# Performance work log

Measured on AMD Instinct MI355X. Metric: run time of the kernel, lower is better.

The kernel has to match this reference:

```python
import jax, jax.numpy as jnp
import numpy as np

_EPS = 1e-12  # torch F.normalize eps


def _normalize(x):
    # x: [B, N, 3]; matches torch.nn.functional.normalize(x, dim=2)
    norm = jnp.linalg.norm(x, axis=2, keepdims=True)
    return x / jnp.maximum(norm, _EPS)


def setup_inputs() -> dict:
    key = jax.random.key(0)
    k1, k2 = jax.random.split(key)
    xyz1 = jax.random.normal(k1, (8, 4096, 6), dtype=jnp.float32)
    xyz2 = jax.random.normal(k2, (8, 4096, 6), dtype=jnp.float32)
    return {"xyz1": xyz1, "xyz2": xyz2}


def reference(xyz1, xyz2):
    p1 = xyz1[:, :, :3]  # [B, N, 3]
    p2 = xyz2[:, :, :3]  # [B, M, 3]
    n1 = xyz1[:, :, 3:]  # [B, N, 3]
    n2 = xyz2[:, :, 3:]  # [B, M, 3]

    # Pairwise squared L2: |a|^2 + |b|^2 - 2 a.b  -> [B, N, M]
    sq1 = jnp.sum(p1 * p1, axis=2)  # [B, N]
    sq2 = jnp.sum(p2 * p2, axis=2)  # [B, M]
    cross = jnp.einsum('bnd,bmd->bnm', p1, p2)
    d = sq1[:, :, None] + sq2[:, None, :] - 2.0 * cross  # [B, N, M]

    dist1 = jnp.min(d, axis=2)      # [B, N] NN of each p1 in p2
    idx1 = jnp.argmin(d, axis=2)    # [B, N]
    dist2 = jnp.min(d, axis=1)      # [B, M] NN of each p2 in p1
    idx2 = jnp.argmin(d, axis=1)    # [B, M]

    # Gather matched normals
    t1 = jnp.take_along_axis(n2, idx1[:, :, None], axis=1)  # [B, N, 3]
    t2 = jnp.take_along_axis(n1, idx2[:, :, None], axis=1)  # [B, M, 3]

    nd1 = jnp.sum((_normalize(n1) - _normalize(t1)) ** 2, axis=2)  # [B, N]
    nd2 = jnp.sum((_normalize(n2) - _normalize(t2)) ** 2, axis=2)  # [B, M]

    return jnp.mean(dist1) + jnp.mean(dist2) + jnp.mean(nd1) + jnp.mean(nd2)
```

## Files before the change

### kernel.cpp

```cpp
#include <hip/hip_runtime.h>
#include <cstdint>

#define NB 8
#define NP 4096
#define NDB 16
#define THREADS 256
#define Q 8
#define CHUNK (THREADS * Q)
#define NCHUNK (NP / CHUNK)
#define SEG 64
#define TSEG (NP / SEG)


__global__ __launch_bounds__(256) void chamfer_prep(
    const float* __restrict__ xyz1, const float* __restrict__ xyz2,
    float4* __restrict__ pk, float4* __restrict__ nrm)
{
    int gid = blockIdx.x * 256 + threadIdx.x;
    int c = gid >> 15;
    const float* src = (c ? xyz2 : xyz1) + (size_t)(gid & 32767) * 6;
    const float2* s2 = (const float2*)src;
    float2 a = s2[0], bv = s2[1], cv = s2[2];
    float x = a.x, y = a.y, z = bv.x;
    float nx = bv.y, ny = cv.x, nz = cv.y;
    pk[gid] = make_float4(x, y, z, -0.5f * (x * x + y * y + z * z));
    float rn = 1.0f / fmaxf(sqrtf(nx * nx + ny * ny + nz * nz), 1e-12f);
    nrm[gid] = make_float4(nx * rn, ny * rn, nz * rn, 0.0f);
}

__global__ __launch_bounds__(THREADS) void chamfer_argmin(
    const float4* __restrict__ pk, float* __restrict__ scores)
{
    __shared__ float4 tgt[TSEG];

    unsigned int x = blockIdx.x;
    int seg   = x & (SEG - 1);
    int chunk = (x >> 6) & (NCHUNK - 1);
    int db    = x >> 7;
    int b     = db & 7;
    int dir   = db >> 3;
    int qrow  = dir * NB + b;
    int trow  = (1 - dir) * NB + b;

    if (threadIdx.x < TSEG)
        tgt[threadIdx.x] = pk[(size_t)trow * NP + seg * TSEG + threadIdx.x];
    __syncthreads();

    const float4* qp = pk + (size_t)qrow * NP;
    float qx[Q], qy[Q], qz[Q], bs[Q];
    int qbase = chunk * CHUNK + threadIdx.x;
    #pragma unroll
    for (int i = 0; i < Q; ++i) {
        float4 qv = qp[qbase + i * THREADS];
        qx[i] = qv.x; qy[i] = qv.y; qz[i] = qv.z;
        bs[i] = -3.4e38f;
    }

    #pragma unroll 8
    for (int k = 0; k < TSEG; ++k) {
        float4 t = tgt[k];
        #pragma unroll
        for (int i = 0; i < Q; ++i) {
            float s = fmaf(t.x, qx[i], fmaf(t.y, qy[i], fmaf(t.z, qz[i], t.w)));
            bs[i] = fmaxf(bs[i], s);
        }
    }

    float* srow = scores + ((size_t)db * SEG + seg) * NP + qbase;
    #pragma unroll
    for (int i = 0; i < Q; ++i) srow[i * THREADS] = bs[i];
}

__global__ __launch_bounds__(256) void chamfer_finish(
    const float4* __restrict__ pk, const float4* __restrict__ nrm,
    const float* __restrict__ scores, float* __restrict__ out)
{
    int gid = blockIdx.x * 256 + threadIdx.x;
    int q  = gid & (NP - 1);
    int db = gid >> 12;
    int b  = db & 7;
    int dir = db >> 3;
    int qrow = dir * NB + b;
    int trow = (1 - dir) * NB + b;

    const float* sb = scores + (size_t)db * SEG * NP + q;
    float best = -3.4e38f;
    int wseg = 0;
    #pragma unroll
    for (int s = 0; s < SEG; ++s) {
        float v = sb[(size_t)s * NP];
        wseg = (v > best) ? s : wseg;
        best = fmaxf(best, v);
    }

    float4 qv = pk[(size_t)qrow * NP + q];
    const float4* tb = pk + (size_t)trow * NP + wseg * TSEG;
    int jf = -1;
    #pragma unroll 8
    for (int k = 0; k < TSEG; ++k) {
        float4 t = tb[k];
        float s = fmaf(t.x, qv.x, fmaf(t.y, qv.y, fmaf(t.z, qv.z, t.w)));
        bool hit = (s == best) && (jf < 0);
        jf = hit ? k : jf;
    }
    int j = wseg * TSEG + (jf < 0 ? 0 : jf);

    float d = fmaxf(-2.0f * (qv.w + best), 0.0f);

    float4 a = nrm[(size_t)qrow * NP + q];
    float4 t = nrm[(size_t)trow * NP + j];
    float dot = a.x * t.x + a.y * t.y + a.z * t.z;
    float nd = fmaf(-2.0f, dot, 2.0f);

    float contrib = (d + nd) * (1.0f / 32768.0f);
    for (int off = 32; off > 0; off >>= 1)
        contrib += __shfl_down(contrib, off, 64);
    __shared__ float wsum[4];
    if ((threadIdx.x & 63) == 0) wsum[threadIdx.x >> 6] = contrib;
    __syncthreads();
    if (threadIdx.x == 0)
        atomicAdd(out, wsum[0] + wsum[1] + wsum[2] + wsum[3]);
}

extern "C" void kernel_launch(void* const* d_in, const int* in_sizes, int n_in,
                              void* d_out, int out_size, void* d_ws, size_t ws_size,
                              hipStream_t stream) {
    const float* xyz1 = (const float*)d_in[0];
    const float* xyz2 = (const float*)d_in[1];
    char* ws = (char*)d_ws;
    float4* pk     = (float4*)(ws);
    float4* nrm    = (float4*)(ws + (1u << 20));
    float*  scores = (float*)(ws + (2u << 20));

    hipMemsetAsync(d_out, 0, sizeof(float), stream);
    chamfer_prep<<<256, 256, 0, stream>>>(xyz1, xyz2, pk, nrm);
    chamfer_argmin<<<NDB * NCHUNK * SEG, THREADS, 0, stream>>>(pk, scores);
    chamfer_finish<<<(NDB * NP) / 256, 256, 0, stream>>>(pk, nrm, scores, (float*)d_out);
}
```

Before: 96.94 us.

## Use packed FP32 FMA over target pairs and widen per-thread query tile

The argmin kernel now handles two target points per step with v_pk_fma_f32. The targets are rearranged in shared memory into x/y/z/w pairs, and each query is duplicated into float2 registers. Each thread now holds 16 queries instead of 8, which halves the grid to one block per (direction, batch, segment) and doubles reuse of each shared-memory load. The output memset is folded into the prep kernel to drop an API call. The change risks higher register pressure, lower occupancy and a smaller grid (1024 blocks), and packed FMA rounding may break exact equality with the finish kernel's scalar recomputation of the best score.

```diff
diff --git a/kernel.cpp b/kernel.cpp
--- a/kernel.cpp
+++ b/kernel.cpp
@@ -5,18 +5,25 @@
 #define NP 4096
 #define NDB 16
 #define THREADS 256
-#define Q 8
-#define CHUNK (THREADS * Q)
-#define NCHUNK (NP / CHUNK)
+#define Q 16
 #define SEG 64
 #define TSEG (NP / SEG)
+#define NPAIR (TSEG / 2)
 
+
+__device__ inline float2 pk_fma(float2 a, float2 b, float2 c) {
+    float2 d;
+    asm("v_pk_fma_f32 %0, %1, %2, %3"
+        : "=v"(d) : "v"(a), "v"(b), "v"(c));
+    return d;
+}
 
 __global__ __launch_bounds__(256) void chamfer_prep(
     const float* __restrict__ xyz1, const float* __restrict__ xyz2,
-    float4* __restrict__ pk, float4* __restrict__ nrm)
+    float4* __restrict__ pk, float4* __restrict__ nrm, float* __restrict__ out)
 {
     int gid = blockIdx.x * 256 + threadIdx.x;
+    if (gid == 0) *out = 0.0f;
     int c = gid >> 15;
     const float* src = (c ? xyz2 : xyz1) + (size_t)(gid & 32767) * 6;
     const float2* s2 = (const float2*)src;
@@ -31,42 +38,55 @@
 __global__ __launch_bounds__(THREADS) void chamfer_argmin(
     const float4* __restrict__ pk, float* __restrict__ scores)
 {
-    __shared__ float4 tgt[TSEG];
+    __shared__ float tgt[TSEG * 4];
 
     unsigned int x = blockIdx.x;
-    int seg   = x & (SEG - 1);
-    int chunk = (x >> 6) & (NCHUNK - 1);
-    int db    = x >> 7;
-    int b     = db & 7;
-    int dir   = db >> 3;
-    int qrow  = dir * NB + b;
-    int trow  = (1 - dir) * NB + b;
+    int seg = x & (SEG - 1);
+    int db  = x >> 6;
+    int b   = db & 7;
+    int dir = db >> 3;
+    int qrow = dir * NB + b;
+    int trow = (1 - dir) * NB + b;
 
-    if (threadIdx.x < TSEG)
-        tgt[threadIdx.x] = pk[(size_t)trow * NP + seg * TSEG + threadIdx.x];
+    if (threadIdx.x < TSEG) {
+        float4 t = pk[(size_t)trow * NP + seg * TSEG + threadIdx.x];
+        int blk = threadIdx.x >> 1, h = threadIdx.x & 1;
+        float* dstp = tgt + blk * 8 + h;
+        dstp[0] = t.x; dstp[2] = t.y; dstp[4] = t.z; dstp[6] = t.w;
+    }
     __syncthreads();
 
     const float4* qp = pk + (size_t)qrow * NP;
-    float qx[Q], qy[Q], qz[Q], bs[Q];
-    int qbase = chunk * CHUNK + threadIdx.x;
+    float2 qx2[Q], qy2[Q], qz2[Q];
+    float bs[Q];
     #pragma unroll
     for (int i = 0; i < Q; ++i) {
-        float4 qv = qp[qbase + i * THREADS];
-        qx[i] = qv.x; qy[i] = qv.y; qz[i] = qv.z;
+        float4 qv = qp[threadIdx.x + i * THREADS];
+        qx2[i] = make_float2(qv.x, qv.x);
+        qy2[i] = make_float2(qv.y, qv.y);
+        qz2[i] = make_float2(qv.z, qv.z);
         bs[i] = -3.4e38f;
     }
 
-    #pragma unroll 8
-    for (int k = 0; k < TSEG; ++k) {
-        float4 t = tgt[k];
+    const float4* tp = (const float4*)tgt;
+    #pragma unroll 4
+    for (int k = 0; k < NPAIR; ++k) {
+        float4 r0 = tp[2 * k];
+        float4 r1 = tp[2 * k + 1];
+        float2 x01 = make_float2(r0.x, r0.y);
+        float2 y01 = make_float2(r0.z, r0.w);
+        float2 z01 = make_float2(r1.x, r1.y);
+        float2 w01 = make_float2(r1.z, r1.w);
         #pragma unroll
         for (int i = 0; i < Q; ++i) {
-            float s = fmaf(t.x, qx[i], fmaf(t.y, qy[i], fmaf(t.z, qz[i], t.w)));
-            bs[i] = fmaxf(bs[i], s);
+            float2 s01 = pk_fma(x01, qx2[i],
+                          pk_fma(y01, qy2[i],
+                           pk_fma(z01, qz2[i], w01)));
+            bs[i] = fmaxf(fmaxf(bs[i], s01.x), s01.y);
         }
     }
 
-    float* srow = scores + ((size_t)db * SEG + seg) * NP + qbase;
+    float* srow = scores + ((size_t)db * SEG + seg) * NP + threadIdx.x;
     #pragma unroll
     for (int i = 0; i < Q; ++i) srow[i * THREADS] = bs[i];
 }
@@ -132,8 +152,7 @@
     float4* nrm    = (float4*)(ws + (1u << 20));
     float*  scores = (float*)(ws + (2u << 20));
 
-    hipMemsetAsync(d_out, 0, sizeof(float), stream);
-    chamfer_prep<<<256, 256, 0, stream>>>(xyz1, xyz2, pk, nrm);
-    chamfer_argmin<<<NDB * NCHUNK * SEG, THREADS, 0, stream>>>(pk, scores);
+    chamfer_prep<<<256, 256, 0, stream>>>(xyz1, xyz2, pk, nrm, (float*)d_out);
+    chamfer_argmin<<<NDB * SEG, THREADS, 0, stream>>>(pk, scores);
     chamfer_finish<<<(NDB * NP) / 256, 256, 0, stream>>>(pk, nrm, scores, (float*)d_out);
 }
```

New measurement: 98.26 us. No clear change (+1.4%).
